# Optimization experiments

Measured on AMD Instinct MI355X. Metric: run time of the kernel, lower is better.

## Reference

```python
import jax, jax.numpy as jnp
import numpy as np

T, B = 128, 512
OBS_DIM = 512
HIDDEN = 512
ACTION_DIM = 18
LN_EPS = 1e-6  # flax LayerNorm default


def _layer_norm(x, scale, bias):
    m = jnp.mean(x, axis=-1, keepdims=True)
    v = jnp.var(x, axis=-1, keepdims=True)
    return (x - m) * jax.lax.rsqrt(v + LN_EPS) * scale + bias


def setup_inputs() -> dict:
    key = jax.random.key(0)
    ks = jax.random.split(key, 16)
    sc = lambda k, sh: jax.random.normal(k, sh, jnp.float32) * (1.0 / np.sqrt(sh[0]))
    d = {}
    d['hidden'] = jax.random.normal(ks[0], (B, HIDDEN), jnp.float32)
    d['obs'] = jax.random.normal(ks[1], (T, B, OBS_DIM), jnp.float32)
    d['dones'] = jax.random.randint(ks[2], (T, B), 0, 2).astype(bool)
    d['last_acts'] = jax.random.randint(ks[3], (T, B), 0, ACTION_DIM, dtype=jnp.int32)
    in0 = OBS_DIM + ACTION_DIM
    d['w0'] = sc(ks[4], (in0, HIDDEN)); d['b0'] = jnp.zeros((HIDDEN,), jnp.float32)
    d['ln0_s'] = jnp.ones((HIDDEN,), jnp.float32); d['ln0_b'] = jnp.zeros((HIDDEN,), jnp.float32)
    d['w1'] = sc(ks[5], (HIDDEN, HIDDEN)); d['b1'] = jnp.zeros((HIDDEN,), jnp.float32)
    d['ln1_s'] = jnp.ones((HIDDEN,), jnp.float32); d['ln1_b'] = jnp.zeros((HIDDEN,), jnp.float32)
    d['w_ir'] = sc(ks[6], (HIDDEN, HIDDEN)); d['b_ir'] = jnp.zeros((HIDDEN,), jnp.float32)
    d['w_iz'] = sc(ks[7], (HIDDEN, HIDDEN)); d['b_iz'] = jnp.zeros((HIDDEN,), jnp.float32)
    d['w_in'] = sc(ks[8], (HIDDEN, HIDDEN)); d['b_in'] = jnp.zeros((HIDDEN,), jnp.float32)
    d['w_hr'] = sc(ks[9], (HIDDEN, HIDDEN))
    d['w_hz'] = sc(ks[10], (HIDDEN, HIDDEN))
    d['w_hn'] = sc(ks[11], (HIDDEN, HIDDEN)); d['b_hn'] = jnp.zeros((HIDDEN,), jnp.float32)
    d['w_out'] = sc(ks[12], (HIDDEN, ACTION_DIM)); d['b_out'] = jnp.zeros((ACTION_DIM,), jnp.float32)
    return d


def reference(hidden, obs, dones, last_acts,
              w0, b0, ln0_s, ln0_b, w1, b1, ln1_s, ln1_b,
              w_ir, b_ir, w_iz, b_iz, w_in, b_in,
              w_hr, w_hz, w_hn, b_hn, w_out, b_out):
    # embed last actions and concat with obs: [T, B, obs_dim + action_dim]
    one_hot = jax.nn.one_hot(last_acts, ACTION_DIM, dtype=obs.dtype)
    x = jnp.concatenate([obs, one_hot], axis=-1)
    # MLP encoder: Dense -> LayerNorm -> relu, applied over all (T, B) at once
    x = jax.nn.relu(_layer_norm(x @ w0 + b0, ln0_s, ln0_b))
    x = jax.nn.relu(_layer_norm(x @ w1 + b1, ln1_s, ln1_b))

    # ScannedRNN: GRUCell with reset-to-zero carry on done, scanned over time
    def step(h, xs):
        xt, dt = xs  # xt: [B, H], dt: [B] bool
        h = jnp.where(dt[:, None], jnp.zeros_like(h), h)
        r = jax.nn.sigmoid(xt @ w_ir + b_ir + h @ w_hr)
        z = jax.nn.sigmoid(xt @ w_iz + b_iz + h @ w_hz)
        n = jnp.tanh(xt @ w_in + b_in + r * (h @ w_hn + b_hn))
        h_new = (1.0 - z) * n + z * h
        return h_new, h_new

    new_hidden, y = jax.lax.scan(step, hidden, (x, dones))
    q_vals = y @ w_out + b_out  # [T, B, action_dim]
    return new_hidden, q_vals
```

## Files before the change

### kernel.cpp

```cpp
#include <hip/hip_runtime.h>
#include <cstdint>
#include <cstddef>


#define TT 128
#define BBATCH 512
#define HH 512
#define MM 65536
#define AD 18
#define GSTEPS 4

typedef __attribute__((ext_vector_type(8))) short short8;
typedef __attribute__((ext_vector_type(4))) float float4v;
typedef __attribute__((ext_vector_type(4))) unsigned int uint4v;

__device__ __forceinline__ unsigned short f2bf(float f) {
  union { float f; unsigned int u; } v; v.f = f;
  unsigned int r = v.u + 0x7fffu + ((v.u >> 16) & 1u);
  return (unsigned short)(r >> 16);
}
__device__ __forceinline__ float bf2f(unsigned short h) {
  union { unsigned int u; float f; } v; v.u = ((unsigned int)h) << 16;
  return v.f;
}

__device__ __forceinline__ unsigned int load_u32_coh(const unsigned int* p) {
  unsigned int v;
  asm volatile("global_load_dword %0, %1, off sc0 sc1\n\ts_waitcnt vmcnt(0)"
               : "=v"(v) : "v"(p) : "memory");
  return v;
}
__device__ __forceinline__ void store_u32_coh(unsigned int* p, unsigned int v) {
  asm volatile("global_store_dword %0, %1, off sc0 sc1"
               :: "v"(p), "v"(v) : "memory");
}
__device__ __forceinline__ void store_u64_coh(void* p, unsigned long long v) {
  asm volatile("global_store_dwordx2 %0, %1, off sc0 sc1"
               :: "v"(p), "v"(v) : "memory");
}

typedef __attribute__((address_space(3))) unsigned int* lds_u32p;
typedef const __attribute__((address_space(1))) unsigned int* glb_u32p;
__device__ __forceinline__ void async16(void* lds, const void* g) {
  __builtin_amdgcn_global_load_lds(
      (glb_u32p)(unsigned long long)g,
      (lds_u32p)(unsigned int)(unsigned long long)lds, 16, 0, 0);
}


__global__ __launch_bounds__(256) void k_conv_obs(
    const float* __restrict__ src, unsigned short* __restrict__ dst,
    unsigned int* __restrict__ flag) {
  if (blockIdx.x == 0 && threadIdx.x == 0) *flag = 0u;
  int i = blockIdx.x * 256 + threadIdx.x;
  float4v v = ((const float4v*)src)[i];
  unsigned long long pk = (unsigned long long)f2bf(v[0])
      | ((unsigned long long)f2bf(v[1]) << 16)
      | ((unsigned long long)f2bf(v[2]) << 32)
      | ((unsigned long long)f2bf(v[3]) << 48);
  ((unsigned long long*)dst)[i] = pk;
}

__global__ __launch_bounds__(256) void k_prep_t(
    const float* __restrict__ w0, const float* __restrict__ w1,
    const float* __restrict__ wir, const float* __restrict__ wiz,
    const float* __restrict__ win,
    unsigned short* __restrict__ W0at, unsigned short* __restrict__ W1t,
    unsigned short* __restrict__ Wit) {
  int o = blockIdx.x * 256 + threadIdx.x;
  int n = o >> 9, k = o & 511;
  int z = blockIdx.y;
  const float* s = (z == 0) ? w0 : (z == 1) ? w1 : (z == 2) ? wir
                 : (z == 3) ? wiz : win;
  unsigned short b = f2bf(s[k * 512 + n]);
  if (z == 0) W0at[o] = b;
  else if (z == 1) W1t[o] = b;
  else Wit[(size_t)(z - 2) * 262144 + o] = b;
}

__global__ __launch_bounds__(256) void k_prep_whf(
    const float* __restrict__ whr, const float* __restrict__ whz,
    const float* __restrict__ whn, unsigned short* __restrict__ Whf) {
  int i = blockIdx.x * 256 + threadIdx.x;
  int k = i / 1536, n = i - k * 1536;
  const float* s = (n < 512) ? whr : (n < 1024) ? whz : whn;
  float v = s[k * 512 + (n & 511)];
  Whf[((size_t)(k >> 3) * 1536 + n) * 8 + (k & 7)] = f2bf(v);
}

__global__ __launch_bounds__(256) void k_prep_misc(
    const float* __restrict__ w0, const float* __restrict__ bir,
    const float* __restrict__ biz, const float* __restrict__ bin,
    const float* __restrict__ wout, const float* __restrict__ hidden,
    const int* __restrict__ dI,
    unsigned short* __restrict__ w0act, float* __restrict__ gib,
    unsigned short* __restrict__ WoutT, unsigned short* __restrict__ hbuf,
    unsigned int* __restrict__ ready, unsigned int* __restrict__ flag) {
  int i = blockIdx.x * 256 + threadIdx.x;
  if (i < 9216) {
    int a = i >> 9, n = i & 511;
    w0act[i] = f2bf(w0[(512 + a) * 512 + n]);
  }
  if (i < 1536)
    gib[i] = (i < 512) ? bir[i] : (i < 1024) ? biz[i - 512] : bin[i - 1024];
  if (i < 32768) {
    int n = i >> 9, k = i & 511;
    WoutT[i] = f2bf(n < AD ? wout[k * AD + n] : 0.f);
  }
  if (i < 262144) hbuf[i] = f2bf(hidden[i]);
  if (i < 33280) ready[i] = 0u;
  if (i < 16384) { if (dI[i] & 0xFFFFFFFE) atomicOr(flag, 1u); }
}


template <int MODE>
__global__ __launch_bounds__(256) void k_gemm_bt(
    const unsigned short* __restrict__ Ab,
    const unsigned short* __restrict__ Btb,
    unsigned short* __restrict__ Cb,
    int Ndim, const float* __restrict__ bias,
    const unsigned short* __restrict__ gW,
    const int* __restrict__ acts) {
  __shared__ unsigned short As[4096];
  __shared__ unsigned short Bs[4096];
  const int tid = threadIdx.x, wave = tid >> 6, lane = tid & 63;
  const int quad = lane >> 4, l15 = lane & 15;
  const int m0 = blockIdx.x * 128, n0 = blockIdx.y * 128;
  const int mblk = (wave & 1) * 64, nblk = (wave >> 1) * 64;

  float4v acc[4][4];
#pragma unroll
  for (int a = 0; a < 4; ++a)
#pragma unroll
    for (int b = 0; b < 4; ++b) acc[a][b] = (float4v){0.f, 0.f, 0.f, 0.f};

  for (int k0 = 0; k0 < 512; k0 += 32) {
#pragma unroll
    for (int r = 0; r < 2; ++r) {
      int u = r * 256 + wave * 64 + lane;
      int ch = u >> 7, mm = u & 127;
      async16(&As[(size_t)(r * 256 + wave * 64) * 8],
              Ab + (size_t)(m0 + mm) * 512 + k0 + ch * 8);
      async16(&Bs[(size_t)(r * 256 + wave * 64) * 8],
              Btb + (size_t)(n0 + mm) * 512 + k0 + ch * 8);
    }
    __syncthreads();
    short8 afr[4], bfr[4];
#pragma unroll
    for (int mi = 0; mi < 4; ++mi)
      afr[mi] = *(const short8*)&As[((quad << 7) + mblk + mi * 16 + l15) * 8];
#pragma unroll
    for (int ni = 0; ni < 4; ++ni)
      bfr[ni] = *(const short8*)&Bs[((quad << 7) + nblk + ni * 16 + l15) * 8];
#pragma unroll
    for (int mi = 0; mi < 4; ++mi)
#pragma unroll
      for (int ni = 0; ni < 4; ++ni)
        acc[mi][ni] = __builtin_amdgcn_mfma_f32_16x16x32_bf16(
            afr[mi], bfr[ni], acc[mi][ni], 0, 0, 0);
    __syncthreads();
  }

#pragma unroll
  for (int mi = 0; mi < 4; ++mi) {
#pragma unroll
    for (int i = 0; i < 4; ++i) {
      int row = m0 + mblk + mi * 16 + quad * 4 + i;
      int arow = (MODE == 1) ? acts[row] : 0;
#pragma unroll
      for (int ni = 0; ni < 4; ++ni) {
        int col = n0 + nblk + ni * 16 + l15;
        float v = acc[mi][ni][i] + bias[col];
        if (MODE == 1) v += bf2f(gW[arow * 512 + col]);
        Cb[(size_t)row * Ndim + col] = f2bf(v);
      }
    }
  }
}


__global__ __launch_bounds__(256) void k_ln_relu(
    const unsigned short* __restrict__ X, unsigned short* __restrict__ Y,
    const float* __restrict__ sc, const float* __restrict__ bi) {
  int row = blockIdx.x * 4 + (threadIdx.x >> 6);
  int lane = threadIdx.x & 63;
  uint4v u = *(const uint4v*)(X + (size_t)row * 512 + lane * 8);
  float v[8];
#pragma unroll
  for (int j = 0; j < 4; ++j) {
    v[2 * j] = bf2f((unsigned short)(u[j] & 0xffffu));
    v[2 * j + 1] = bf2f((unsigned short)(u[j] >> 16));
  }
  float s = 0.f, q = 0.f;
#pragma unroll
  for (int j = 0; j < 8; ++j) { s += v[j]; q += v[j] * v[j]; }
#pragma unroll
  for (int d = 1; d < 64; d <<= 1) {
    s += __shfl_xor(s, d, 64);
    q += __shfl_xor(q, d, 64);
  }
  float mean = s * (1.f / 512.f);
  float var = fmaxf(q * (1.f / 512.f) - mean * mean, 0.f);
  float rstd = rsqrtf(var + 1e-6f);
  float4v s0 = *(const float4v*)(sc + lane * 8);
  float4v s1 = *(const float4v*)(sc + lane * 8 + 4);
  float4v c0 = *(const float4v*)(bi + lane * 8);
  float4v c1 = *(const float4v*)(bi + lane * 8 + 4);
  uint4v w;
#pragma unroll
  for (int j = 0; j < 4; ++j) {
    float a0 = fmaxf((v[2 * j] - mean) * rstd * (j < 2 ? s0[2 * j] : s1[2 * j - 4])
                         + (j < 2 ? c0[2 * j] : c1[2 * j - 4]), 0.f);
    float a1 = fmaxf((v[2 * j + 1] - mean) * rstd
                         * (j < 2 ? s0[2 * j + 1] : s1[2 * j - 3])
                         + (j < 2 ? c0[2 * j + 1] : c1[2 * j - 3]), 0.f);
    w[j] = (unsigned int)f2bf(a0) | ((unsigned int)f2bf(a1) << 16);
  }
  *(uint4v*)(Y + (size_t)row * 512 + lane * 8) = w;
}


__global__ __launch_bounds__(256, 1) void k_gru(
    const unsigned short* __restrict__ Whf, const unsigned short* __restrict__ gin,
    const float* __restrict__ bhn, const int* __restrict__ dI,
    const unsigned char* __restrict__ dB, const unsigned int* __restrict__ flag,
    const unsigned short* __restrict__ hbuf, unsigned short* __restrict__ ybuf,
    float* __restrict__ outh, unsigned int* __restrict__ ready) {
  __shared__ __align__(16) unsigned short gin_lds[2][GSTEPS * 3 * 64 * 16];
  __shared__ unsigned char d_lds[TT * 64];

  const int tid = threadIdx.x, wave = tid >> 6, lane = tid & 63;
  const int quad = lane >> 4, l15 = lane & 15;
  const int rt = blockIdx.x & 7;
  const int cc = blockIdx.x >> 3;
  const int r0b = rt * 64;
  const int rowb = wave * 16 + l15;
  const int row = r0b + rowb;
  const int c0 = cc * 16 + quad * 4;
  const int bytemode = (int)(*flag);
  const float4v bhn4 = *(const float4v*)(bhn + c0);

  auto stage_gin = [&](int buf, int t0) {
#pragma unroll
    for (int r = 0; r < 6; ++r) {
      int u = r * 256 + tid;
      int half = u & 1;
      int v = u >> 1;
      int rr = v & 63;
      int v2 = v >> 6;
      int g = v2 % 3, s = v2 / 3;
      const unsigned short* src = gin
          + ((size_t)(t0 + s) * 512 + r0b + rr) * 1536 + g * 512 + cc * 16
          + half * 8;
      async16(&gin_lds[buf][(size_t)(r * 256 + wave * 64) * 8], src);
    }
  };

  stage_gin(0, 0);
#pragma unroll
  for (int r = 0; r < 32; ++r) {
    int idx = r * 256 + tid;
    int t = idx >> 6, rr = idx & 63;
    int gidx = t * 512 + r0b + rr;
    d_lds[idx] = bytemode ? dB[gidx] : (unsigned char)(dI[gidx] != 0);
  }

  short8 bw[3][16];
#pragma unroll
  for (int kc = 0; kc < 16; ++kc)
#pragma unroll
    for (int g = 0; g < 3; ++g) {
      size_t u = (size_t)(kc * 4 + quad) * 1536 + (g * 512 + cc * 16 + l15);
      bw[g][kc] = *(const short8*)(Whf + u * 8);
    }

  float hprev[4];
  {
    unsigned long long w = *(const unsigned long long*)(hbuf + (size_t)row * 512 + c0);
#pragma unroll
    for (int i = 0; i < 4; ++i) hprev[i] = bf2f((unsigned short)(w >> (16 * i)));
  }

  __syncthreads();

  const unsigned short* apOffBase = nullptr;  (void)apOffBase;

  for (int t = 0; t < TT; ++t) {
    if (t > 0) {
      if (wave == 0) {
        const unsigned int* fp =
            ready + ((size_t)rt * 130 + t) * 32 + (lane & 31);
        unsigned int v;
        int guard = 0;
        do {
          v = load_u32_coh(fp);
        } while (__ballot(v == 0u) != 0ull && ++guard < (1 << 22));
      }
      __syncthreads();
      asm volatile("" ::: "memory");
    }

    const unsigned short* hsrc =
        (t == 0) ? hbuf : ybuf + (size_t)(t - 1) * 262144;
    const unsigned short* ap = hsrc + (size_t)row * 512 + quad * 8;
    short8 af[16];
#pragma unroll
    for (int kc = 0; kc < 16; ++kc) af[kc] = *(const short8*)(ap + kc * 32);

    const int dd = (int)d_lds[(t << 6) + rowb];
    if (dd) {
      const short8 z8 = {0, 0, 0, 0, 0, 0, 0, 0};
#pragma unroll
      for (int kc = 0; kc < 16; ++kc) af[kc] = z8;
    }

    if ((t & (GSTEPS - 1)) == 0 && t + GSTEPS < TT)
      stage_gin(((t >> 2) + 1) & 1, t + GSTEPS);

    const int sl = t & (GSTEPS - 1), bufc = (t >> 2) & 1;
    float gr[4], gz[4], gn[4];
    {
      const unsigned short* gl =
          &gin_lds[bufc][((size_t)(sl * 3) * 64 + rowb) * 16 + quad * 4];
      unsigned long long w0 = *(const unsigned long long*)(gl);
      unsigned long long w1 = *(const unsigned long long*)(gl + 1024);
      unsigned long long w2 = *(const unsigned long long*)(gl + 2048);
#pragma unroll
      for (int i = 0; i < 4; ++i) {
        gr[i] = bf2f((unsigned short)(w0 >> (16 * i)));
        gz[i] = bf2f((unsigned short)(w1 >> (16 * i)));
        gn[i] = bf2f((unsigned short)(w2 >> (16 * i)));
      }
    }

    float4v a0 = {0.f, 0.f, 0.f, 0.f}, a1 = a0, a2 = a0;
#pragma unroll
    for (int kc = 0; kc < 16; ++kc) {
      a0 = __builtin_amdgcn_mfma_f32_16x16x32_bf16(bw[0][kc], af[kc], a0, 0, 0, 0);
      a1 = __builtin_amdgcn_mfma_f32_16x16x32_bf16(bw[1][kc], af[kc], a1, 0, 0, 0);
      a2 = __builtin_amdgcn_mfma_f32_16x16x32_bf16(bw[2][kc], af[kc], a2, 0, 0, 0);
    }

    unsigned short* ydst = ybuf + (size_t)t * 262144;
    float hv[4];
#pragma unroll
    for (int i = 0; i < 4; ++i) {
      float hold = dd ? 0.f : hprev[i];
      float r = 1.f / (1.f + __expf(-(a0[i] + gr[i])));
      float z = 1.f / (1.f + __expf(-(a1[i] + gz[i])));
      float npre = gn[i] + r * (a2[i] + bhn4[i]);
      float n = 1.f - 2.f / (1.f + __expf(2.f * npre));
      hv[i] = (1.f - z) * n + z * hold;
      hprev[i] = hv[i];
    }
    {
      unsigned long long pk = (unsigned long long)f2bf(hv[0])
          | ((unsigned long long)f2bf(hv[1]) << 16)
          | ((unsigned long long)f2bf(hv[2]) << 32)
          | ((unsigned long long)f2bf(hv[3]) << 48);
      store_u64_coh(ydst + (size_t)row * 512 + c0, pk);
    }
    if (t == TT - 1) {
      float4v o = {hv[0], hv[1], hv[2], hv[3]};
      *(float4v*)(outh + (size_t)row * 512 + c0) = o;
    }

    __syncthreads();
    if (tid == 0)
      store_u32_coh(&ready[((size_t)rt * 130 + t + 1) * 32 + cc], 1u);
  }
}


__global__ __launch_bounds__(256) void k_qout(
    const unsigned short* __restrict__ Yb, const unsigned short* __restrict__ Wt,
    const float* __restrict__ bout, float* __restrict__ Q) {
  __shared__ unsigned short As[4096];
  __shared__ unsigned short Bs[2048];
  const int tid = threadIdx.x, wave = tid >> 6, lane = tid & 63;
  const int quad = lane >> 4, l15 = lane & 15;
  const int m0 = blockIdx.x * 128;

  float4v acc[2][4];
#pragma unroll
  for (int a = 0; a < 2; ++a)
#pragma unroll
    for (int b = 0; b < 4; ++b) acc[a][b] = (float4v){0.f, 0.f, 0.f, 0.f};

  for (int k0 = 0; k0 < 512; k0 += 32) {
#pragma unroll
    for (int r = 0; r < 2; ++r) {
      int u = r * 256 + wave * 64 + lane;
      int ch = u >> 7, mm = u & 127;
      async16(&As[(size_t)(r * 256 + wave * 64) * 8],
              Yb + (size_t)(m0 + mm) * 512 + k0 + ch * 8);
    }
    {
      int u = wave * 64 + lane;
      int ch = u >> 6, nn = u & 63;
      async16(&Bs[(size_t)(wave * 64) * 8], Wt + (size_t)nn * 512 + k0 + ch * 8);
    }
    __syncthreads();
    short8 afr[2], bfr[4];
#pragma unroll
    for (int mi = 0; mi < 2; ++mi)
      afr[mi] = *(const short8*)&As[((quad << 7) + wave * 32 + mi * 16 + l15) * 8];
#pragma unroll
    for (int ni = 0; ni < 4; ++ni)
      bfr[ni] = *(const short8*)&Bs[((quad << 6) + ni * 16 + l15) * 8];
#pragma unroll
    for (int mi = 0; mi < 2; ++mi)
#pragma unroll
      for (int ni = 0; ni < 4; ++ni)
        acc[mi][ni] = __builtin_amdgcn_mfma_f32_16x16x32_bf16(
            afr[mi], bfr[ni], acc[mi][ni], 0, 0, 0);
    __syncthreads();
  }
#pragma unroll
  for (int mi = 0; mi < 2; ++mi)
#pragma unroll
    for (int ni = 0; ni < 4; ++ni)
#pragma unroll
      for (int i = 0; i < 4; ++i) {
        int row = m0 + wave * 32 + mi * 16 + quad * 4 + i;
        int colq = ni * 16 + l15;
        if (colq < AD) Q[(size_t)row * AD + colq] = acc[mi][ni][i] + bout[colq];
      }
}


extern "C" void kernel_launch(void* const* d_in, const int* in_sizes, int n_in,
                              void* d_out, int out_size, void* d_ws,
                              size_t ws_size, hipStream_t stream) {
  const float* hidden = (const float*)d_in[0];
  const float* obs = (const float*)d_in[1];
  const void* dones = d_in[2];
  const int* acts = (const int*)d_in[3];
  const float* w0 = (const float*)d_in[4];
  const float* b0 = (const float*)d_in[5];
  const float* ln0s = (const float*)d_in[6];
  const float* ln0b = (const float*)d_in[7];
  const float* w1 = (const float*)d_in[8];
  const float* b1 = (const float*)d_in[9];
  const float* ln1s = (const float*)d_in[10];
  const float* ln1b = (const float*)d_in[11];
  const float* wir = (const float*)d_in[12];
  const float* bir = (const float*)d_in[13];
  const float* wiz = (const float*)d_in[14];
  const float* biz = (const float*)d_in[15];
  const float* win = (const float*)d_in[16];
  const float* bin = (const float*)d_in[17];
  const float* whr = (const float*)d_in[18];
  const float* whz = (const float*)d_in[19];
  const float* whn = (const float*)d_in[20];
  const float* bhn = (const float*)d_in[21];
  const float* wout = (const float*)d_in[22];
  const float* bout = (const float*)d_in[23];

  char* ws = (char*)d_ws;
  unsigned short* bufA = (unsigned short*)(ws);
  unsigned short* bufB = (unsigned short*)(ws + 67108864ULL);
  unsigned short* gin = (unsigned short*)(ws + 134217728ULL);
  char* D = ws + 134217728ULL + 201326592ULL;
  unsigned short* W0at = (unsigned short*)(D);
  unsigned short* W1t = (unsigned short*)(D + 524288);
  unsigned short* Wit = (unsigned short*)(D + 1048576);
  unsigned short* Whf = (unsigned short*)(D + 2621440);
  unsigned short* WoutT = (unsigned short*)(D + 4194304);
  unsigned short* w0act = (unsigned short*)(D + 4259840);
  float* gib = (float*)(D + 4292608);
  unsigned short* hbuf = (unsigned short*)(D + 4300800);
  unsigned int* ready = (unsigned int*)(D + 5349376);
  unsigned int* flag = ready + 33280;

  (void)in_sizes; (void)n_in; (void)out_size; (void)ws_size;

  k_conv_obs<<<32768, 256, 0, stream>>>(obs, bufA, flag);
  k_prep_t<<<dim3(1024, 5), 256, 0, stream>>>(w0, w1, wir, wiz, win, W0at, W1t, Wit);
  k_prep_whf<<<3072, 256, 0, stream>>>(whr, whz, whn, Whf);
  k_prep_misc<<<1024, 256, 0, stream>>>(w0, bir, biz, bin, wout, hidden,
                                        (const int*)dones, w0act, gib, WoutT,
                                        hbuf, ready, flag);
  k_gemm_bt<1><<<dim3(512, 4), 256, 0, stream>>>(bufA, W0at, bufB, 512, b0, w0act, acts);
  k_ln_relu<<<16384, 256, 0, stream>>>(bufB, bufA, ln0s, ln0b);
  k_gemm_bt<0><<<dim3(512, 4), 256, 0, stream>>>(bufA, W1t, bufB, 512, b1, nullptr, nullptr);
  k_ln_relu<<<16384, 256, 0, stream>>>(bufB, bufA, ln1s, ln1b);
  k_gemm_bt<0><<<dim3(512, 12), 256, 0, stream>>>(bufA, Wit, gin, 1536, gib, nullptr, nullptr);
  k_gru<<<256, 256, 0, stream>>>(Whf, gin, bhn, (const int*)dones,
                                 (const unsigned char*)dones, flag, hbuf, bufB,
                                 (float*)d_out, ready);
  k_qout<<<512, 256, 0, stream>>>(bufB, WoutT, bout, (float*)d_out + 262144);
}
```

Before: 1.312 ms.

## Pre-tile GRU input gates per block, deepen staging, pad ready flags

The input-gate GEMM now writes its output in a blocked layout so that each GRU workgroup's slice for a timestep is contiguous, and the staging copy becomes a straight linear async copy. The staging depth doubles from 4 to 8 timesteps. Each ready flag is padded to its own 128-byte stride to avoid false sharing while spinning, and the flag array is moved into the freed bufA region with a separate zeroing kernel. This costs a scattered store pattern in the GEMM epilogue and one extra small kernel launch.

```diff
diff --git a/kernel.cpp b/kernel.cpp
--- a/kernel.cpp
+++ b/kernel.cpp
@@ -8,7 +8,9 @@
 #define HH 512
 #define MM 65536
 #define AD 18
-#define GSTEPS 4
+#define GSTEPS 8
+#define FSTRIDE 32
+#define READY_U32 1064960
 
 typedef __attribute__((ext_vector_type(8))) short short8;
 typedef __attribute__((ext_vector_type(4))) float float4v;
@@ -95,7 +97,7 @@
     const int* __restrict__ dI,
     unsigned short* __restrict__ w0act, float* __restrict__ gib,
     unsigned short* __restrict__ WoutT, unsigned short* __restrict__ hbuf,
-    unsigned int* __restrict__ ready, unsigned int* __restrict__ flag) {
+    unsigned int* __restrict__ flag) {
   int i = blockIdx.x * 256 + threadIdx.x;
   if (i < 9216) {
     int a = i >> 9, n = i & 511;
@@ -108,8 +110,12 @@
     WoutT[i] = f2bf(n < AD ? wout[k * AD + n] : 0.f);
   }
   if (i < 262144) hbuf[i] = f2bf(hidden[i]);
-  if (i < 33280) ready[i] = 0u;
   if (i < 16384) { if (dI[i] & 0xFFFFFFFE) atomicOr(flag, 1u); }
+}
+
+__global__ __launch_bounds__(256) void k_zero(unsigned int* __restrict__ p) {
+  int i = (blockIdx.x * 256 + threadIdx.x) * 4;
+  if (i < READY_U32) *(uint4v*)(p + i) = (uint4v){0u, 0u, 0u, 0u};
 }
 
 
@@ -172,7 +178,15 @@
         int col = n0 + nblk + ni * 16 + l15;
         float v = acc[mi][ni][i] + bias[col];
         if (MODE == 1) v += bf2f(gW[arow * 512 + col]);
-        Cb[(size_t)row * Ndim + col] = f2bf(v);
+        if (MODE == 2) {
+          int t = row >> 9, b = row & 511;
+          int c = col & 511;
+          size_t dst = ((size_t)((b >> 6) * 32 + (c >> 4)) * 128 + t) * 3072
+                     + (size_t)(col >> 9) * 1024 + (b & 63) * 16 + (c & 15);
+          Cb[dst] = f2bf(v);
+        } else {
+          Cb[(size_t)row * Ndim + col] = f2bf(v);
+        }
       }
     }
   }
@@ -240,19 +254,14 @@
   const int bytemode = (int)(*flag);
   const float4v bhn4 = *(const float4v*)(bhn + c0);
 
+  const unsigned short* gsrc = gin + (size_t)(rt * 32 + cc) * 128 * 3072;
+
   auto stage_gin = [&](int buf, int t0) {
-#pragma unroll
-    for (int r = 0; r < 6; ++r) {
-      int u = r * 256 + tid;
-      int half = u & 1;
-      int v = u >> 1;
-      int rr = v & 63;
-      int v2 = v >> 6;
-      int g = v2 % 3, s = v2 / 3;
-      const unsigned short* src = gin
-          + ((size_t)(t0 + s) * 512 + r0b + rr) * 1536 + g * 512 + cc * 16
-          + half * 8;
-      async16(&gin_lds[buf][(size_t)(r * 256 + wave * 64) * 8], src);
+    const unsigned short* src = gsrc + (size_t)t0 * 3072;
+#pragma unroll
+    for (int r = 0; r < 12; ++r) {
+      async16(&gin_lds[buf][(size_t)(r * 256 + wave * 64) * 8],
+              src + (size_t)(r * 256 + tid) * 8);
     }
   };
 
@@ -283,13 +292,11 @@
 
   __syncthreads();
 
-  const unsigned short* apOffBase = nullptr;  (void)apOffBase;
-
   for (int t = 0; t < TT; ++t) {
     if (t > 0) {
       if (wave == 0) {
         const unsigned int* fp =
-            ready + ((size_t)rt * 130 + t) * 32 + (lane & 31);
+            ready + (((size_t)rt * 130 + t) * 32 + (lane & 31)) * FSTRIDE;
         unsigned int v;
         int guard = 0;
         do {
@@ -315,9 +322,9 @@
     }
 
     if ((t & (GSTEPS - 1)) == 0 && t + GSTEPS < TT)
-      stage_gin(((t >> 2) + 1) & 1, t + GSTEPS);
-
-    const int sl = t & (GSTEPS - 1), bufc = (t >> 2) & 1;
+      stage_gin(((t >> 3) + 1) & 1, t + GSTEPS);
+
+    const int sl = t & (GSTEPS - 1), bufc = (t >> 3) & 1;
     float gr[4], gz[4], gn[4];
     {
       const unsigned short* gl =
@@ -367,7 +374,7 @@
 
     __syncthreads();
     if (tid == 0)
-      store_u32_coh(&ready[((size_t)rt * 130 + t + 1) * 32 + cc], 1u);
+      store_u32_coh(&ready[(((size_t)rt * 130 + t + 1) * 32 + cc) * FSTRIDE], 1u);
   }
 }
 
@@ -470,8 +477,8 @@
   unsigned short* w0act = (unsigned short*)(D + 4259840);
   float* gib = (float*)(D + 4292608);
   unsigned short* hbuf = (unsigned short*)(D + 4300800);
-  unsigned int* ready = (unsigned int*)(D + 5349376);
-  unsigned int* flag = ready + 33280;
+  unsigned int* flag = (unsigned int*)(D + 4825088);
+  unsigned int* ready = (unsigned int*)ws;
 
   (void)in_sizes; (void)n_in; (void)out_size; (void)ws_size;
 
@@ -480,12 +487,13 @@
   k_prep_whf<<<3072, 256, 0, stream>>>(whr, whz, whn, Whf);
   k_prep_misc<<<1024, 256, 0, stream>>>(w0, bir, biz, bin, wout, hidden,
                                         (const int*)dones, w0act, gib, WoutT,
-                                        hbuf, ready, flag);
+                                        hbuf, flag);
   k_gemm_bt<1><<<dim3(512, 4), 256, 0, stream>>>(bufA, W0at, bufB, 512, b0, w0act, acts);
   k_ln_relu<<<16384, 256, 0, stream>>>(bufB, bufA, ln0s, ln0b);
   k_gemm_bt<0><<<dim3(512, 4), 256, 0, stream>>>(bufA, W1t, bufB, 512, b1, nullptr, nullptr);
   k_ln_relu<<<16384, 256, 0, stream>>>(bufB, bufA, ln1s, ln1b);
-  k_gemm_bt<0><<<dim3(512, 12), 256, 0, stream>>>(bufA, Wit, gin, 1536, gib, nullptr, nullptr);
+  k_gemm_bt<2><<<dim3(512, 12), 256, 0, stream>>>(bufA, Wit, gin, 1536, gib, nullptr, nullptr);
+  k_zero<<<1041, 256, 0, stream>>>(ready);
   k_gru<<<256, 256, 0, stream>>>(Whf, gin, bhn, (const int*)dones,
                                  (const unsigned char*)dones, flag, hbuf, bufB,
                                  (float*)d_out, ready);
```

New measurement: 1.239 ms. -5.6%, faster.
